# Optimization experiments

Measured on AMD Instinct MI355X. Metric: run time of the kernel, lower is better.

The kernel has to match this reference:

```python
import jax, jax.numpy as jnp
import numpy as np

HIDDEN = 512
NUM_HEADS = 8


def setup_inputs() -> dict:
    key = jax.random.key(0)
    ks = jax.random.split(key, 8)
    Tq, Tk, Cq, Ck, H = 1, 65536, 512, 512, HIDDEN
    s = 1.0 / np.sqrt(H)
    return {
        "Q": jax.random.normal(ks[0], (Tq, Cq), jnp.float32),
        "K": jax.random.normal(ks[1], (Tk, Ck), jnp.float32),
        "Wq": jax.random.normal(ks[2], (H, Cq), jnp.float32) * s,
        "bq": jax.random.normal(ks[3], (H,), jnp.float32) * s,
        "Wk": jax.random.normal(ks[4], (H, Ck), jnp.float32) * s,
        "bk": jax.random.normal(ks[5], (H,), jnp.float32) * s,
        "Wout": jax.random.normal(ks[6], (1, NUM_HEADS), jnp.float32) * 0.3,
        "bout": jax.random.normal(ks[7], (1,), jnp.float32) * 0.3,
    }


def reference(Q, K, Wq, bq, Wk, bk, Wout, bout):
    h = NUM_HEADS
    H = Wq.shape[0]
    d = H // h  # per-head dim
    # linear + ReLU projections
    Ql = jax.nn.relu(Q @ Wq.T + bq)          # [1, H]
    Kl = jax.nn.relu(K @ Wk.T + bk)          # [Tk, H]
    # split into heads (T_q == 1 is required by linear_out)
    Qh = Ql.reshape(h, d)                    # [h, d]
    Kh = Kl.reshape(-1, h, d)                # [Tk, h, d]
    # per-head scores, scaled by sqrt(d_head); dropout rate 0 -> identity
    scores = jnp.einsum('hd,thd->th', Qh, Kh) / (d ** 0.5)  # [Tk, h]
    # learned per-head fusion, then softmax over the T_k axis
    logits = scores @ Wout.T + bout          # [Tk, 1]
    return jax.nn.softmax(logits, axis=0)    # [Tk, 1]
```

## Files before the change

### kernel.cpp

```cpp
#include <hip/hip_runtime.h>
#include <hip/hip_fp16.h>

#define CDIM  512
#define ROWS  65536
#define NWG   128
#define TILES 16

typedef _Float16 half8  __attribute__((ext_vector_type(8)));
typedef _Float16 half4t __attribute__((ext_vector_type(4)));
typedef float    f32x16 __attribute__((ext_vector_type(16)));

__global__ void qproj_kernel(const float* __restrict__ Q, const float* __restrict__ Wq,
                             const float* __restrict__ bq, const float* __restrict__ Wout,
                             float* __restrict__ v) {
    __shared__ float qs[CDIM];
    const int t = threadIdx.x;
    qs[t] = Q[t]; qs[t + 256] = Q[t + 256];
    __syncthreads();
    const int jj  = t >> 4;
    const int sub = t & 15;
    const int j   = blockIdx.x * 16 + jj;
    const float4* w4 = (const float4*)(Wq + (size_t)j * CDIM + sub * 32);
    const float4* q4 = (const float4*)(qs + sub * 32);
    float s = 0.f;
    #pragma unroll
    for (int i = 0; i < 8; ++i) {
        float4 w = w4[i]; float4 q = q4[i];
        s = fmaf(w.x, q.x, s); s = fmaf(w.y, q.y, s);
        s = fmaf(w.z, q.z, s); s = fmaf(w.w, q.w, s);
    }
    s += __shfl_xor(s, 1); s += __shfl_xor(s, 2);
    s += __shfl_xor(s, 4); s += __shfl_xor(s, 8);
    if (sub == 0) {
        s += bq[j];
        s = fmaxf(s, 0.f);
        v[j] = s * Wout[j >> 6] * 0.125f;
    }
}

__global__ void wkfrag_kernel(const float* __restrict__ Wk, _Float16* __restrict__ Wkf) {
    const int gid = blockIdx.x * 256 + threadIdx.x;
    const int jb  = gid >> 11;
    const int kc  = (gid >> 6) & 31;
    const int l   = gid & 63;
    const int j   = jb * 32 + (l & 31);
    const int k   = kc * 16 + (l >> 5) * 8;
    const float* src = Wk + (size_t)j * CDIM + k;
    float4 f0 = *(const float4*)(src);
    float4 f1 = *(const float4*)(src + 4);
    half8 h;
    h[0]=(_Float16)f0.x; h[1]=(_Float16)f0.y; h[2]=(_Float16)f0.z; h[3]=(_Float16)f0.w;
    h[4]=(_Float16)f1.x; h[5]=(_Float16)f1.y; h[6]=(_Float16)f1.z; h[7]=(_Float16)f1.w;
    *(half8*)(Wkf + (size_t)gid * 8) = h;
}

__global__ __launch_bounds__(512, 2) void score_kernel(
    const float* __restrict__ Kmat, const _Float16* __restrict__ Wkf,
    const float* __restrict__ bk, const float* __restrict__ v,
    float* __restrict__ partial2)
{
    __shared__ alignas(16) char stage[2][32768];
    __shared__ float scratch[2][8][32];

    const int tid  = threadIdx.x;
    const int lane = tid & 63;
    const int wave = tid >> 6;
    const int l31  = lane & 31;
    const int lhi  = lane >> 5;
    const int cls  = blockIdx.y;
    const int jb   = cls * 8 + wave;

    half8 B[32];
    const half8* bsrc = (const half8*)Wkf + ((size_t)jb * 32) * 64 + lane;
    #pragma unroll
    for (int kc = 0; kc < 32; ++kc) B[kc] = bsrc[kc * 64];
    const int jmy = jb * 32 + l31;
    const float bj = bk[jmy];
    const float vj = v[jmy];

    const int rowbase0 = blockIdx.x * (TILES * 32);
    float* pbase = partial2 + (size_t)cls * ROWS;

    const int sw  = tid & 127;
    const int skc = sw >> 2;
    const int skh = (sw >> 1) & 1;
    const int spr = sw & 1;
    const int srow_off = tid >> 7;

    #pragma unroll
    for (int it = 0; it < 8; ++it) {
        const int row = it * 4 + srow_off;
        float4 g = *(const float4*)(Kmat + (size_t)(rowbase0 + row) * CDIM + sw * 4);
        half4t h = {(_Float16)g.x, (_Float16)g.y, (_Float16)g.z, (_Float16)g.w};
        const int off = skc * 1024 + (((row + 32 * skh + skc) & 63) * 16) + spr * 8;
        *(half4t*)(&stage[0][off]) = h;
    }
    __syncthreads();

    for (int t = 0; t < TILES; ++t) {
        const int cur = t & 1;
        const bool pf = (t + 1 < TILES);

        float4 g[8];
        if (pf) {
            const int rs = rowbase0 + (t + 1) * 32;
            #pragma unroll
            for (int it = 0; it < 8; ++it)
                g[it] = *(const float4*)(Kmat + (size_t)(rs + it * 4 + srow_off) * CDIM + sw * 4);
        }

        if (t > 0 && tid < 32) {
            float s = 0.f;
            #pragma unroll
            for (int w = 0; w < 8; ++w) s += scratch[(t - 1) & 1][w][tid];
            pbase[rowbase0 + (t - 1) * 32 + tid] = s;
        }

        f32x16 acc0, acc1;
        #pragma unroll
        for (int r = 0; r < 16; ++r) { acc0[r] = 0.f; acc1[r] = 0.f; }
        #pragma unroll
        for (int kc = 0; kc < 32; kc += 2) {
            half8 a0 = *(const half8*)(&stage[cur][kc * 1024 + ((lane + kc) & 63) * 16]);
            half8 a1 = *(const half8*)(&stage[cur][(kc + 1) * 1024 + ((lane + kc + 1) & 63) * 16]);
            acc0 = __builtin_amdgcn_mfma_f32_32x32x16_f16(a0, B[kc],     acc0, 0, 0, 0);
            acc1 = __builtin_amdgcn_mfma_f32_32x32x16_f16(a1, B[kc + 1], acc1, 0, 0, 0);
        }

        float part[16];
        #pragma unroll
        for (int r = 0; r < 16; ++r) {
            float x = fmaxf(acc0[r] + acc1[r] + bj, 0.f) * vj;
            x += __shfl_xor(x, 1);
            x += __shfl_xor(x, 2);
            x += __shfl_xor(x, 4);
            x += __shfl_xor(x, 8);
            x += __shfl_xor(x, 16);
            part[r] = x;
        }
        if (l31 == 0) {
            #pragma unroll
            for (int r = 0; r < 16; ++r)
                scratch[cur][wave][(r & 3) + 8 * (r >> 2) + 4 * lhi] = part[r];
        }

        if (pf) {
            #pragma unroll
            for (int it = 0; it < 8; ++it) {
                const int row = it * 4 + srow_off;
                half4t h = {(_Float16)g[it].x, (_Float16)g[it].y, (_Float16)g[it].z, (_Float16)g[it].w};
                const int off = skc * 1024 + (((row + 32 * skh + skc) & 63) * 16) + spr * 8;
                *(half4t*)(&stage[cur ^ 1][off]) = h;
            }
        }
        __syncthreads();
    }

    if (tid < 32) {
        float s = 0.f;
        #pragma unroll
        for (int w = 0; w < 8; ++w) s += scratch[(TILES - 1) & 1][w][tid];
        pbase[rowbase0 + (TILES - 1) * 32 + tid] = s;
    }
}

__global__ void expsum_kernel(const float* __restrict__ partial2, float* __restrict__ logits,
                              float* __restrict__ blocksum) {
    __shared__ float red[256];
    const int t = threadIdx.x;
    const int row = blockIdx.x * 256 + t;
    const float lg = partial2[row] + partial2[ROWS + row];
    logits[row] = lg;
    red[t] = expf(lg);
    __syncthreads();
    for (int s = 128; s > 0; s >>= 1) {
        if (t < s) red[t] += red[t + s];
        __syncthreads();
    }
    if (t == 0) blocksum[blockIdx.x] = red[0];
}

__global__ void norm_kernel(const float* __restrict__ logits, const float* __restrict__ blocksum,
                            float* __restrict__ out) {
    __shared__ float red[256];
    const int t = threadIdx.x;
    red[t] = blocksum[t];
    __syncthreads();
    for (int s = 128; s > 0; s >>= 1) {
        if (t < s) red[t] += red[t + s];
        __syncthreads();
    }
    const float zinv = 1.0f / red[0];
    const int i = blockIdx.x * 256 + t;
    out[i] = expf(logits[i]) * zinv;
}

extern "C" void kernel_launch(void* const* d_in, const int* in_sizes, int n_in,
                              void* d_out, int out_size, void* d_ws, size_t ws_size,
                              hipStream_t stream) {
    const float* Q    = (const float*)d_in[0];
    const float* Kmat = (const float*)d_in[1];
    const float* Wq   = (const float*)d_in[2];
    const float* bq   = (const float*)d_in[3];
    const float* Wk   = (const float*)d_in[4];
    const float* bk   = (const float*)d_in[5];
    const float* Wout = (const float*)d_in[6];
    float* out = (float*)d_out;

    char* ws = (char*)d_ws;
    _Float16* Wkf   = (_Float16*)(ws);
    float* v        = (float*)(ws + 524288);
    float* partial2 = (float*)(ws + 526336);
    float* logits   = (float*)(ws + 1050624);
    float* blocksum = (float*)(ws + 1312768);

    hipLaunchKernelGGL(qproj_kernel,  dim3(32),       dim3(256), 0, stream, Q, Wq, bq, Wout, v);
    hipLaunchKernelGGL(wkfrag_kernel, dim3(128),      dim3(256), 0, stream, Wk, Wkf);
    hipLaunchKernelGGL(score_kernel,  dim3(NWG, 2),   dim3(512), 0, stream, Kmat, Wkf, bk, v, partial2);
    hipLaunchKernelGGL(expsum_kernel, dim3(256),      dim3(256), 0, stream, partial2, logits, blocksum);
    hipLaunchKernelGGL(norm_kernel,   dim3(256),      dim3(256), 0, stream, logits, blocksum, out);
}
```

Before: 75.92 us.

## Stream fp32 K tiles directly into LDS via global_load_lds, convert at read

The score kernel's K-tile staging now uses 16-byte global_load_lds transfers that write fp32 rows straight into an XOR-swizzled shared-memory buffer. This replaces the old path of loading into registers, converting to fp16 and storing to LDS. Conversion to fp16 moves to the MFMA operand read, using packed round-toward-zero converts. The aim is to cut register pressure and VALU/LDS-store work in the prefetch path and let the async copy overlap with compute. In exchange, shared memory per block doubles to about 128KB, which limits occupancy to one block per CU, and LDS read traffic per MFMA doubles.

```diff
diff --git a/kernel.cpp b/kernel.cpp
--- a/kernel.cpp
+++ b/kernel.cpp
@@ -7,8 +7,12 @@
 #define TILES 16
 
 typedef _Float16 half8  __attribute__((ext_vector_type(8)));
-typedef _Float16 half4t __attribute__((ext_vector_type(4)));
+typedef __fp16   fp16x2 __attribute__((ext_vector_type(2)));
 typedef float    f32x16 __attribute__((ext_vector_type(16)));
+
+#define GLD_LDS16(gp, lp) __builtin_amdgcn_global_load_lds( \
+    (const __attribute__((address_space(1))) unsigned int*)(gp), \
+    (__attribute__((address_space(3))) unsigned int*)(lp), 16, 0, 0)
 
 __global__ void qproj_kernel(const float* __restrict__ Q, const float* __restrict__ Wq,
                              const float* __restrict__ bq, const float* __restrict__ Wout,
@@ -59,7 +63,7 @@
     const float* __restrict__ bk, const float* __restrict__ v,
     float* __restrict__ partial2)
 {
-    __shared__ alignas(16) char stage[2][32768];
+    __shared__ alignas(16) float stage[2][32 * 512];
     __shared__ float scratch[2][8][32];
 
     const int tid  = threadIdx.x;
@@ -81,32 +85,34 @@
     const int rowbase0 = blockIdx.x * (TILES * 32);
     float* pbase = partial2 + (size_t)cls * ROWS;
 
-    const int sw  = tid & 127;
-    const int skc = sw >> 2;
-    const int skh = (sw >> 1) & 1;
-    const int spr = sw & 1;
-    const int srow_off = tid >> 7;
-
-    #pragma unroll
-    for (int it = 0; it < 8; ++it) {
-        const int row = it * 4 + srow_off;
-        float4 g = *(const float4*)(Kmat + (size_t)(rowbase0 + row) * CDIM + sw * 4);
-        half4t h = {(_Float16)g.x, (_Float16)g.y, (_Float16)g.z, (_Float16)g.w};
-        const int off = skc * 1024 + (((row + 32 * skh + skc) & 63) * 16) + spr * 8;
-        *(half4t*)(&stage[0][off]) = h;
+    const int srow = wave >> 1;
+    const int scol = (wave & 1) << 6;
+
+    {
+        const float* tb = Kmat + (size_t)rowbase0 * CDIM;
+        #pragma unroll
+        for (int it = 0; it < 8; ++it) {
+            const int r = it * 4 + srow;
+            const int c = (scol + lane) ^ r;
+            GLD_LDS16(tb + (size_t)r * CDIM + c * 4,
+                      &stage[0][(it * 512 + wave * 64) * 4]);
+        }
     }
     __syncthreads();
 
     for (int t = 0; t < TILES; ++t) {
         const int cur = t & 1;
-        const bool pf = (t + 1 < TILES);
-
-        float4 g[8];
-        if (pf) {
-            const int rs = rowbase0 + (t + 1) * 32;
+
+        if (t + 1 < TILES) {
+            const float* tb = Kmat + (size_t)(rowbase0 + (t + 1) * 32) * CDIM;
+            float* db = &stage[cur ^ 1][0];
             #pragma unroll
-            for (int it = 0; it < 8; ++it)
-                g[it] = *(const float4*)(Kmat + (size_t)(rs + it * 4 + srow_off) * CDIM + sw * 4);
+            for (int it = 0; it < 8; ++it) {
+                const int r = it * 4 + srow;
+                const int c = (scol + lane) ^ r;
+                GLD_LDS16(tb + (size_t)r * CDIM + c * 4,
+                          db + (it * 512 + wave * 64) * 4);
+            }
         }
 
         if (t > 0 && tid < 32) {
@@ -116,15 +122,29 @@
             pbase[rowbase0 + (t - 1) * 32 + tid] = s;
         }
 
+        const float* sb = &stage[cur][0];
         f32x16 acc0, acc1;
         #pragma unroll
         for (int r = 0; r < 16; ++r) { acc0[r] = 0.f; acc1[r] = 0.f; }
         #pragma unroll
         for (int kc = 0; kc < 32; kc += 2) {
-            half8 a0 = *(const half8*)(&stage[cur][kc * 1024 + ((lane + kc) & 63) * 16]);
-            half8 a1 = *(const half8*)(&stage[cur][(kc + 1) * 1024 + ((lane + kc + 1) & 63) * 16]);
-            acc0 = __builtin_amdgcn_mfma_f32_32x32x16_f16(a0, B[kc],     acc0, 0, 0, 0);
-            acc1 = __builtin_amdgcn_mfma_f32_32x32x16_f16(a1, B[kc + 1], acc1, 0, 0, 0);
+            const int cb0 = kc * 4 + lhi * 2;
+            const int cb1 = cb0 + 4;
+            float4 f00 = *(const float4*)(sb + ((l31 * 128 + ((cb0    ) ^ l31)) << 2));
+            float4 f01 = *(const float4*)(sb + ((l31 * 128 + ((cb0 + 1) ^ l31)) << 2));
+            float4 f10 = *(const float4*)(sb + ((l31 * 128 + ((cb1    ) ^ l31)) << 2));
+            float4 f11 = *(const float4*)(sb + ((l31 * 128 + ((cb1 + 1) ^ l31)) << 2));
+            union { fp16x2 h2[4]; half8 h8; } u0, u1;
+            u0.h2[0] = __builtin_amdgcn_cvt_pkrtz(f00.x, f00.y);
+            u0.h2[1] = __builtin_amdgcn_cvt_pkrtz(f00.z, f00.w);
+            u0.h2[2] = __builtin_amdgcn_cvt_pkrtz(f01.x, f01.y);
+            u0.h2[3] = __builtin_amdgcn_cvt_pkrtz(f01.z, f01.w);
+            u1.h2[0] = __builtin_amdgcn_cvt_pkrtz(f10.x, f10.y);
+            u1.h2[1] = __builtin_amdgcn_cvt_pkrtz(f10.z, f10.w);
+            u1.h2[2] = __builtin_amdgcn_cvt_pkrtz(f11.x, f11.y);
+            u1.h2[3] = __builtin_amdgcn_cvt_pkrtz(f11.z, f11.w);
+            acc0 = __builtin_amdgcn_mfma_f32_32x32x16_f16(u0.h8, B[kc],     acc0, 0, 0, 0);
+            acc1 = __builtin_amdgcn_mfma_f32_32x32x16_f16(u1.h8, B[kc + 1], acc1, 0, 0, 0);
         }
 
         float part[16];
@@ -144,15 +164,6 @@
                 scratch[cur][wave][(r & 3) + 8 * (r >> 2) + 4 * lhi] = part[r];
         }
 
-        if (pf) {
-            #pragma unroll
-            for (int it = 0; it < 8; ++it) {
-                const int row = it * 4 + srow_off;
-                half4t h = {(_Float16)g[it].x, (_Float16)g[it].y, (_Float16)g[it].z, (_Float16)g[it].w};
-                const int off = skc * 1024 + (((row + 32 * skh + skc) & 63) * 16) + spr * 8;
-                *(half4t*)(&stage[cur ^ 1][off]) = h;
-            }
-        }
         __syncthreads();
     }
 
@@ -214,9 +225,9 @@
     float* logits   = (float*)(ws + 1050624);
     float* blocksum = (float*)(ws + 1312768);
 
-    hipLaunchKernelGGL(qproj_kernel,  dim3(32),       dim3(256), 0, stream, Q, Wq, bq, Wout, v);
-    hipLaunchKernelGGL(wkfrag_kernel, dim3(128),      dim3(256), 0, stream, Wk, Wkf);
-    hipLaunchKernelGGL(score_kernel,  dim3(NWG, 2),   dim3(512), 0, stream, Kmat, Wkf, bk, v, partial2);
-    hipLaunchKernelGGL(expsum_kernel, dim3(256),      dim3(256), 0, stream, partial2, logits, blocksum);
-    hipLaunchKernelGGL(norm_kernel,   dim3(256),      dim3(256), 0, stream, logits, blocksum, out);
-}
+    hipLaunchKernelGGL(qproj_kernel,  dim3(32),     dim3(256), 0, stream, Q, Wq, bq, Wout, v);
+    hipLaunchKernelGGL(wkfrag_kernel, dim3(128),    dim3(256), 0, stream, Wk, Wkf);
+    hipLaunchKernelGGL(score_kernel,  dim3(NWG, 2), dim3(512), 0, stream, Kmat, Wkf, bk, v, partial2);
+    hipLaunchKernelGGL(expsum_kernel, dim3(256),    dim3(256), 0, stream, partial2, logits, blocksum);
+    hipLaunchKernelGGL(norm_kernel,   dim3(256),    dim3(256), 0, stream, logits, blocksum, out);
+}
```

Measured after the change: 107.0 us. 40.9% more time.

## Split score kernel into 4 column groups of 4 waves with row-major swizzled staging

Applied to the files above, without the earlier changes.

Changes the score kernel from 2 column groups of 8 waves to 4 groups of 4 waves (256 threads), so each block handles 128 hidden columns and the K tile is staged 4 times instead of twice. Staging now uses a row-major fp16 layout with XOR swizzle and packed cvt_pkrtz conversion, and the next-tile prefetch is split into two halves interleaved with the MFMA loop using sched barriers. The cross-lane reduction becomes a transpose-style butterfly that needs fewer shuffles. The cost is twice the global K reads and conversions, plus a fourth partial buffer that expsum must add.

```diff
diff --git a/kernel.cpp b/kernel.cpp
--- a/kernel.cpp
+++ b/kernel.cpp
@@ -3,11 +3,12 @@
 
 #define CDIM  512
 #define ROWS  65536
-#define NWG   128
 #define TILES 16
+#define GX    128
+#define NCLS  4
 
 typedef _Float16 half8  __attribute__((ext_vector_type(8)));
-typedef _Float16 half4t __attribute__((ext_vector_type(4)));
+typedef __fp16   fp16x2 __attribute__((ext_vector_type(2)));
 typedef float    f32x16 __attribute__((ext_vector_type(16)));
 
 __global__ void qproj_kernel(const float* __restrict__ Q, const float* __restrict__ Wq,
@@ -54,13 +55,13 @@
     *(half8*)(Wkf + (size_t)gid * 8) = h;
 }
 
-__global__ __launch_bounds__(512, 2) void score_kernel(
+__global__ __launch_bounds__(256, 2) void score_kernel(
     const float* __restrict__ Kmat, const _Float16* __restrict__ Wkf,
     const float* __restrict__ bk, const float* __restrict__ v,
     float* __restrict__ partial2)
 {
-    __shared__ alignas(16) char stage[2][32768];
-    __shared__ float scratch[2][8][32];
+    __shared__ alignas(16) _Float16 stage[2][32][512];
+    __shared__ float scratch2[2][4][32];
 
     const int tid  = threadIdx.x;
     const int lane = tid & 63;
@@ -68,32 +69,34 @@
     const int l31  = lane & 31;
     const int lhi  = lane >> 5;
     const int cls  = blockIdx.y;
-    const int jb   = cls * 8 + wave;
+    const int jb   = cls * 4 + wave;
 
     half8 B[32];
-    const half8* bsrc = (const half8*)Wkf + ((size_t)jb * 32) * 64 + lane;
+    const half8* bsrc = (const half8*)Wkf + (size_t)jb * 2048 + lane;
     #pragma unroll
     for (int kc = 0; kc < 32; ++kc) B[kc] = bsrc[kc * 64];
     const int jmy = jb * 32 + l31;
     const float bj = bk[jmy];
     const float vj = v[jmy];
 
-    const int rowbase0 = blockIdx.x * (TILES * 32);
+    const int rowbase = blockIdx.x * (TILES * 32);
     float* pbase = partial2 + (size_t)cls * ROWS;
 
-    const int sw  = tid & 127;
-    const int skc = sw >> 2;
-    const int skh = (sw >> 1) & 1;
-    const int spr = sw & 1;
-    const int srow_off = tid >> 7;
-
-    #pragma unroll
-    for (int it = 0; it < 8; ++it) {
-        const int row = it * 4 + srow_off;
-        float4 g = *(const float4*)(Kmat + (size_t)(rowbase0 + row) * CDIM + sw * 4);
-        half4t h = {(_Float16)g.x, (_Float16)g.y, (_Float16)g.z, (_Float16)g.w};
-        const int off = skc * 1024 + (((row + 32 * skh + skc) & 63) * 16) + spr * 8;
-        *(half4t*)(&stage[0][off]) = h;
+    {
+        #pragma unroll
+        for (int i = 0; i < 8; ++i) {
+            const int rt = wave * 8 + i;
+            const float* src = Kmat + (size_t)(rowbase + rt) * CDIM + lane * 8;
+            float4 a = *(const float4*)(src);
+            float4 b = *(const float4*)(src + 4);
+            union { fp16x2 h2[4]; half8 h8; } u;
+            u.h2[0] = __builtin_amdgcn_cvt_pkrtz(a.x, a.y);
+            u.h2[1] = __builtin_amdgcn_cvt_pkrtz(a.z, a.w);
+            u.h2[2] = __builtin_amdgcn_cvt_pkrtz(b.x, b.y);
+            u.h2[3] = __builtin_amdgcn_cvt_pkrtz(b.z, b.w);
+            const int slot = lane ^ (rt & 7);
+            *(half8*)(&stage[0][rt][slot * 8]) = u.h8;
+        }
     }
     __syncthreads();
 
@@ -101,66 +104,142 @@
         const int cur = t & 1;
         const bool pf = (t + 1 < TILES);
 
-        float4 g[8];
+        if (t > 0 && tid < 32) {
+            const int pt = (t - 1) & 1;
+            float s = scratch2[pt][0][tid] + scratch2[pt][1][tid]
+                    + scratch2[pt][2][tid] + scratch2[pt][3][tid];
+            pbase[rowbase + (t - 1) * 32 + tid] = s;
+        }
+
+        f32x16 acc0, acc1;
+        #pragma unroll
+        for (int r = 0; r < 16; ++r) { acc0[r] = 0.f; acc1[r] = 0.f; }
+
+        const _Float16* sb = &stage[cur][0][0];
+
+        float4 ga0[4], gb0[4];
         if (pf) {
-            const int rs = rowbase0 + (t + 1) * 32;
+            const int rs = rowbase + (t + 1) * 32;
             #pragma unroll
-            for (int it = 0; it < 8; ++it)
-                g[it] = *(const float4*)(Kmat + (size_t)(rs + it * 4 + srow_off) * CDIM + sw * 4);
-        }
-
-        if (t > 0 && tid < 32) {
-            float s = 0.f;
-            #pragma unroll
-            for (int w = 0; w < 8; ++w) s += scratch[(t - 1) & 1][w][tid];
-            pbase[rowbase0 + (t - 1) * 32 + tid] = s;
-        }
-
-        f32x16 acc0, acc1;
-        #pragma unroll
-        for (int r = 0; r < 16; ++r) { acc0[r] = 0.f; acc1[r] = 0.f; }
-        #pragma unroll
-        for (int kc = 0; kc < 32; kc += 2) {
-            half8 a0 = *(const half8*)(&stage[cur][kc * 1024 + ((lane + kc) & 63) * 16]);
-            half8 a1 = *(const half8*)(&stage[cur][(kc + 1) * 1024 + ((lane + kc + 1) & 63) * 16]);
+            for (int i = 0; i < 4; ++i) {
+                const float* src = Kmat + (size_t)(rs + wave * 8 + i) * CDIM + lane * 8;
+                ga0[i] = *(const float4*)(src);
+                gb0[i] = *(const float4*)(src + 4);
+            }
+        }
+        __builtin_amdgcn_sched_barrier(0);
+
+        #pragma unroll
+        for (int kc = 0; kc < 16; kc += 2) {
+            const int ch0 = (kc * 2 + lhi) ^ (l31 & 7);
+            const int ch1 = ((kc + 1) * 2 + lhi) ^ (l31 & 7);
+            half8 a0 = *(const half8*)(sb + l31 * 512 + ch0 * 8);
+            half8 a1 = *(const half8*)(sb + l31 * 512 + ch1 * 8);
             acc0 = __builtin_amdgcn_mfma_f32_32x32x16_f16(a0, B[kc],     acc0, 0, 0, 0);
             acc1 = __builtin_amdgcn_mfma_f32_32x32x16_f16(a1, B[kc + 1], acc1, 0, 0, 0);
         }
 
-        float part[16];
-        #pragma unroll
-        for (int r = 0; r < 16; ++r) {
-            float x = fmaxf(acc0[r] + acc1[r] + bj, 0.f) * vj;
-            x += __shfl_xor(x, 1);
-            x += __shfl_xor(x, 2);
-            x += __shfl_xor(x, 4);
-            x += __shfl_xor(x, 8);
-            x += __shfl_xor(x, 16);
-            part[r] = x;
-        }
-        if (l31 == 0) {
-            #pragma unroll
-            for (int r = 0; r < 16; ++r)
-                scratch[cur][wave][(r & 3) + 8 * (r >> 2) + 4 * lhi] = part[r];
-        }
-
         if (pf) {
             #pragma unroll
-            for (int it = 0; it < 8; ++it) {
-                const int row = it * 4 + srow_off;
-                half4t h = {(_Float16)g[it].x, (_Float16)g[it].y, (_Float16)g[it].z, (_Float16)g[it].w};
-                const int off = skc * 1024 + (((row + 32 * skh + skc) & 63) * 16) + spr * 8;
-                *(half4t*)(&stage[cur ^ 1][off]) = h;
+            for (int i = 0; i < 4; ++i) {
+                const int rt = wave * 8 + i;
+                union { fp16x2 h2[4]; half8 h8; } u;
+                u.h2[0] = __builtin_amdgcn_cvt_pkrtz(ga0[i].x, ga0[i].y);
+                u.h2[1] = __builtin_amdgcn_cvt_pkrtz(ga0[i].z, ga0[i].w);
+                u.h2[2] = __builtin_amdgcn_cvt_pkrtz(gb0[i].x, gb0[i].y);
+                u.h2[3] = __builtin_amdgcn_cvt_pkrtz(gb0[i].z, gb0[i].w);
+                const int slot = lane ^ (rt & 7);
+                *(half8*)(&stage[cur ^ 1][rt][slot * 8]) = u.h8;
             }
         }
+
+        float4 ga1[4], gb1[4];
+        if (pf) {
+            const int rs = rowbase + (t + 1) * 32;
+            #pragma unroll
+            for (int i = 0; i < 4; ++i) {
+                const float* src = Kmat + (size_t)(rs + wave * 8 + 4 + i) * CDIM + lane * 8;
+                ga1[i] = *(const float4*)(src);
+                gb1[i] = *(const float4*)(src + 4);
+            }
+        }
+        __builtin_amdgcn_sched_barrier(0);
+
+        #pragma unroll
+        for (int kc = 16; kc < 32; kc += 2) {
+            const int ch0 = (kc * 2 + lhi) ^ (l31 & 7);
+            const int ch1 = ((kc + 1) * 2 + lhi) ^ (l31 & 7);
+            half8 a0 = *(const half8*)(sb + l31 * 512 + ch0 * 8);
+            half8 a1 = *(const half8*)(sb + l31 * 512 + ch1 * 8);
+            acc0 = __builtin_amdgcn_mfma_f32_32x32x16_f16(a0, B[kc],     acc0, 0, 0, 0);
+            acc1 = __builtin_amdgcn_mfma_f32_32x32x16_f16(a1, B[kc + 1], acc1, 0, 0, 0);
+        }
+
+        if (pf) {
+            #pragma unroll
+            for (int i = 0; i < 4; ++i) {
+                const int rt = wave * 8 + 4 + i;
+                union { fp16x2 h2[4]; half8 h8; } u;
+                u.h2[0] = __builtin_amdgcn_cvt_pkrtz(ga1[i].x, ga1[i].y);
+                u.h2[1] = __builtin_amdgcn_cvt_pkrtz(ga1[i].z, ga1[i].w);
+                u.h2[2] = __builtin_amdgcn_cvt_pkrtz(gb1[i].x, gb1[i].y);
+                u.h2[3] = __builtin_amdgcn_cvt_pkrtz(gb1[i].z, gb1[i].w);
+                const int slot = lane ^ (rt & 7);
+                *(half8*)(&stage[cur ^ 1][rt][slot * 8]) = u.h8;
+            }
+        }
+
+        float x[16];
+        #pragma unroll
+        for (int r = 0; r < 16; ++r)
+            x[r] = fmaxf(acc0[r] + acc1[r] + bj, 0.f) * vj;
+
+        float q0[8];
+        #pragma unroll
+        for (int i = 0; i < 8; ++i) {
+            const bool b = lane & 1;
+            float keep = b ? x[i + 8] : x[i];
+            float send = b ? x[i] : x[i + 8];
+            q0[i] = keep + __shfl_xor(send, 1);
+        }
+        float q1[4];
+        #pragma unroll
+        for (int i = 0; i < 4; ++i) {
+            const bool b = lane & 2;
+            float keep = b ? q0[i + 4] : q0[i];
+            float send = b ? q0[i] : q0[i + 4];
+            q1[i] = keep + __shfl_xor(send, 2);
+        }
+        float q2[2];
+        #pragma unroll
+        for (int i = 0; i < 2; ++i) {
+            const bool b = lane & 4;
+            float keep = b ? q1[i + 2] : q1[i];
+            float send = b ? q1[i] : q1[i + 2];
+            q2[i] = keep + __shfl_xor(send, 4);
+        }
+        float q3;
+        {
+            const bool b = lane & 8;
+            float keep = b ? q2[1] : q2[0];
+            float send = b ? q2[0] : q2[1];
+            q3 = keep + __shfl_xor(send, 8);
+        }
+        float s = q3 + __shfl_xor(q3, 16);
+        if (l31 < 16) {
+            const int r   = ((l31 & 1) << 3) | ((l31 & 2) << 1) | ((l31 & 4) >> 1) | ((l31 & 8) >> 3);
+            const int row = (r & 3) + 8 * (r >> 2) + 4 * lhi;
+            scratch2[cur][wave][row] = s;
+        }
+
         __syncthreads();
     }
 
     if (tid < 32) {
-        float s = 0.f;
-        #pragma unroll
-        for (int w = 0; w < 8; ++w) s += scratch[(TILES - 1) & 1][w][tid];
-        pbase[rowbase0 + (TILES - 1) * 32 + tid] = s;
+        const int pt = (TILES - 1) & 1;
+        float s = scratch2[pt][0][tid] + scratch2[pt][1][tid]
+                + scratch2[pt][2][tid] + scratch2[pt][3][tid];
+        pbase[rowbase + (TILES - 1) * 32 + tid] = s;
     }
 }
 
@@ -169,7 +248,8 @@
     __shared__ float red[256];
     const int t = threadIdx.x;
     const int row = blockIdx.x * 256 + t;
-    const float lg = partial2[row] + partial2[ROWS + row];
+    const float lg = partial2[row] + partial2[ROWS + row]
+                   + partial2[2 * ROWS + row] + partial2[3 * ROWS + row];
     logits[row] = lg;
     red[t] = expf(lg);
     __syncthreads();
@@ -211,12 +291,12 @@
     _Float16* Wkf   = (_Float16*)(ws);
     float* v        = (float*)(ws + 524288);
     float* partial2 = (float*)(ws + 526336);
-    float* logits   = (float*)(ws + 1050624);
-    float* blocksum = (float*)(ws + 1312768);
-
-    hipLaunchKernelGGL(qproj_kernel,  dim3(32),       dim3(256), 0, stream, Q, Wq, bq, Wout, v);
-    hipLaunchKernelGGL(wkfrag_kernel, dim3(128),      dim3(256), 0, stream, Wk, Wkf);
-    hipLaunchKernelGGL(score_kernel,  dim3(NWG, 2),   dim3(512), 0, stream, Kmat, Wkf, bk, v, partial2);
-    hipLaunchKernelGGL(expsum_kernel, dim3(256),      dim3(256), 0, stream, partial2, logits, blocksum);
-    hipLaunchKernelGGL(norm_kernel,   dim3(256),      dim3(256), 0, stream, logits, blocksum, out);
-}
+    float* logits   = (float*)(ws + 1574912);
+    float* blocksum = (float*)(ws + 1837056);
+
+    hipLaunchKernelGGL(qproj_kernel,  dim3(32),        dim3(256), 0, stream, Q, Wq, bq, Wout, v);
+    hipLaunchKernelGGL(wkfrag_kernel, dim3(128),       dim3(256), 0, stream, Wk, Wkf);
+    hipLaunchKernelGGL(score_kernel,  dim3(GX, NCLS),  dim3(256), 0, stream, Kmat, Wkf, bk, v, partial2);
+    hipLaunchKernelGGL(expsum_kernel, dim3(256),       dim3(256), 0, stream, partial2, logits, blocksum);
+    hipLaunchKernelGGL(norm_kernel,   dim3(256),       dim3(256), 0, stream, logits, blocksum, out);
+}
```

New measurement: 64.43 us. 15.1% less time.

## Hold K rows in registers and stream Wk fragments through LDS via direct loads

Applied to the files above, without the earlier changes.

Restructures the score kernel so each wave keeps 32 rows of converted K as MFMA A-operands in registers and swaps 64KB halves of the fp16 Wk fragment matrix into LDS with global_load_lds, instead of keeping Wk in registers and staging K tiles through LDS. Each block now handles 512 rows for one 256-column half, so each wave processes 64 rows in two passes and alternates Wk halves to reuse what is already loaded. The per-row shuffle reduction becomes a transposing butterfly tree that needs fewer shuffles, and fp32-to-fp16 conversion uses packed cvt_pkrtz. The cost is 128KB of LDS per block, which limits occupancy, plus round-toward-zero conversion and less overlap between K loads and compute.

```diff
diff --git a/kernel.cpp b/kernel.cpp
--- a/kernel.cpp
+++ b/kernel.cpp
@@ -1,14 +1,25 @@
 #include <hip/hip_runtime.h>
 #include <hip/hip_fp16.h>
 
-#define CDIM  512
-#define ROWS  65536
-#define NWG   128
-#define TILES 16
+#define CDIM 512
+#define ROWS 65536
 
 typedef _Float16 half8  __attribute__((ext_vector_type(8)));
-typedef _Float16 half4t __attribute__((ext_vector_type(4)));
+typedef __fp16   fp16x2 __attribute__((ext_vector_type(2)));
 typedef float    f32x16 __attribute__((ext_vector_type(16)));
+
+#define GLD_LDS16(gp, lp) __builtin_amdgcn_global_load_lds( \
+    (const __attribute__((address_space(1))) unsigned int*)(gp), \
+    (__attribute__((address_space(3))) unsigned int*)(lp), 16, 0, 0)
+
+__device__ __forceinline__ half8 cvt8(float4 f0, float4 f1) {
+    union { fp16x2 h2[4]; half8 h8; } u;
+    u.h2[0] = __builtin_amdgcn_cvt_pkrtz(f0.x, f0.y);
+    u.h2[1] = __builtin_amdgcn_cvt_pkrtz(f0.z, f0.w);
+    u.h2[2] = __builtin_amdgcn_cvt_pkrtz(f1.x, f1.y);
+    u.h2[3] = __builtin_amdgcn_cvt_pkrtz(f1.z, f1.w);
+    return u.h8;
+}
 
 __global__ void qproj_kernel(const float* __restrict__ Q, const float* __restrict__ Wq,
                              const float* __restrict__ bq, const float* __restrict__ Wout,
@@ -48,10 +59,7 @@
     const float* src = Wk + (size_t)j * CDIM + k;
     float4 f0 = *(const float4*)(src);
     float4 f1 = *(const float4*)(src + 4);
-    half8 h;
-    h[0]=(_Float16)f0.x; h[1]=(_Float16)f0.y; h[2]=(_Float16)f0.z; h[3]=(_Float16)f0.w;
-    h[4]=(_Float16)f1.x; h[5]=(_Float16)f1.y; h[6]=(_Float16)f1.z; h[7]=(_Float16)f1.w;
-    *(half8*)(Wkf + (size_t)gid * 8) = h;
+    *(half8*)(Wkf + (size_t)gid * 8) = cvt8(f0, f1);
 }
 
 __global__ __launch_bounds__(512, 2) void score_kernel(
@@ -59,109 +67,115 @@
     const float* __restrict__ bk, const float* __restrict__ v,
     float* __restrict__ partial2)
 {
-    __shared__ alignas(16) char stage[2][32768];
-    __shared__ float scratch[2][8][32];
+    __shared__ alignas(16) char Blds[131072];
 
     const int tid  = threadIdx.x;
     const int lane = tid & 63;
     const int wave = tid >> 6;
     const int l31  = lane & 31;
     const int lhi  = lane >> 5;
-    const int cls  = blockIdx.y;
-    const int jb   = cls * 8 + wave;
-
-    half8 B[32];
-    const half8* bsrc = (const half8*)Wkf + ((size_t)jb * 32) * 64 + lane;
+    const int bid  = blockIdx.x;
+    const int cls  = bid & 1;
+    const int rowblock = bid >> 1;
+
+    const int wrow = rowblock * 512 + wave * 64;
+    float* pbase = partial2 + (size_t)cls * ROWS;
+
+    const char* wkf0 = (const char*)Wkf + (size_t)(cls * 8 + 0) * 32768;
+    const char* wkf1 = (const char*)Wkf + (size_t)(cls * 8 + 4) * 32768;
+
+#define SWAPB(src) { \
+    _Pragma("unroll") for (int i = 0; i < 16; ++i) \
+        GLD_LDS16((src) + (size_t)i * 8192 + tid * 16, Blds + i * 8192 + tid * 16); }
+
+    half8 a[32];
+#define LOADA(rb) { \
+    const float* ab = Kmat + (size_t)((rb) + l31) * CDIM + lhi * 8;       \
+    _Pragma("unroll") for (int g = 0; g < 8; ++g) {                        \
+        float4 f[8];                                                       \
+        _Pragma("unroll") for (int q = 0; q < 4; ++q) {                    \
+            f[2*q]   = *(const float4*)(ab + (g*4+q) * 16);                \
+            f[2*q+1] = *(const float4*)(ab + (g*4+q) * 16 + 4);            \
+        }                                                                  \
+        _Pragma("unroll") for (int q = 0; q < 4; ++q)                      \
+            a[g*4+q] = cvt8(f[2*q], f[2*q+1]);                             \
+    } }
+
+    float part[16];
+
+#define DOPHASE(h) { \
+    for (int jbl = 0; jbl < 4; ++jbl) {                                             \
+        const int jg = cls * 256 + (h) * 128 + jbl * 32 + l31;                      \
+        const float bj = bk[jg];                                                    \
+        const float vj = v[jg];                                                     \
+        f32x16 acc0, acc1;                                                          \
+        _Pragma("unroll") for (int r = 0; r < 16; ++r) { acc0[r] = 0.f; acc1[r] = 0.f; } \
+        _Pragma("unroll") for (int kc = 0; kc < 32; kc += 2) {                      \
+            half8 b0 = *(const half8*)(Blds + (((jbl*32 + kc    ) * 64 + lane) << 4)); \
+            half8 b1 = *(const half8*)(Blds + (((jbl*32 + kc + 1) * 64 + lane) << 4)); \
+            acc0 = __builtin_amdgcn_mfma_f32_32x32x16_f16(a[kc],     b0, acc0, 0, 0, 0); \
+            acc1 = __builtin_amdgcn_mfma_f32_32x32x16_f16(a[kc + 1], b1, acc1, 0, 0, 0); \
+        }                                                                           \
+        _Pragma("unroll") for (int r = 0; r < 16; ++r)                              \
+            part[r] += fmaxf(acc0[r] + acc1[r] + bj, 0.f) * vj;                     \
+    } }
+
+#define TREESTORE(dst) { \
+    float q0[8];                                                                    \
+    _Pragma("unroll") for (int i = 0; i < 8; ++i) {                                 \
+        const bool b = lane & 1;                                                    \
+        float keep = b ? part[i + 8] : part[i];                                     \
+        float send = b ? part[i] : part[i + 8];                                     \
+        q0[i] = keep + __shfl_xor(send, 1);                                         \
+    }                                                                               \
+    float q1[4];                                                                    \
+    _Pragma("unroll") for (int i = 0; i < 4; ++i) {                                 \
+        const bool b = lane & 2;                                                    \
+        float keep = b ? q0[i + 4] : q0[i];                                         \
+        float send = b ? q0[i] : q0[i + 4];                                         \
+        q1[i] = keep + __shfl_xor(send, 2);                                         \
+    }                                                                               \
+    float q2[2];                                                                    \
+    _Pragma("unroll") for (int i = 0; i < 2; ++i) {                                 \
+        const bool b = lane & 4;                                                    \
+        float keep = b ? q1[i + 2] : q1[i];                                         \
+        float send = b ? q1[i] : q1[i + 2];                                         \
+        q2[i] = keep + __shfl_xor(send, 4);                                         \
+    }                                                                               \
+    float q3;                                                                       \
+    { const bool b = lane & 8;                                                      \
+      float keep = b ? q2[1] : q2[0];                                               \
+      float send = b ? q2[0] : q2[1];                                               \
+      q3 = keep + __shfl_xor(send, 8); }                                            \
+    float s = q3 + __shfl_xor(q3, 16);                                              \
+    if (l31 < 16) {                                                                 \
+        const int rr  = ((l31 & 1) << 3) | ((l31 & 2) << 1) | ((l31 & 4) >> 1) | ((l31 & 8) >> 3); \
+        const int row = (rr & 3) + 8 * (rr >> 2) + 4 * lhi;                         \
+        (dst)[row] = s;                                                             \
+    } }
+
+    SWAPB(wkf0);
+    LOADA(wrow);
+    __syncthreads();
+
     #pragma unroll
-    for (int kc = 0; kc < 32; ++kc) B[kc] = bsrc[kc * 64];
-    const int jmy = jb * 32 + l31;
-    const float bj = bk[jmy];
-    const float vj = v[jmy];
-
-    const int rowbase0 = blockIdx.x * (TILES * 32);
-    float* pbase = partial2 + (size_t)cls * ROWS;
-
-    const int sw  = tid & 127;
-    const int skc = sw >> 2;
-    const int skh = (sw >> 1) & 1;
-    const int spr = sw & 1;
-    const int srow_off = tid >> 7;
-
+    for (int r = 0; r < 16; ++r) part[r] = 0.f;
+    DOPHASE(0);
+    __syncthreads();
+    SWAPB(wkf1);
+    __syncthreads();
+    DOPHASE(1);
+    TREESTORE(pbase + wrow);
+
+    LOADA(wrow + 32);
     #pragma unroll
-    for (int it = 0; it < 8; ++it) {
-        const int row = it * 4 + srow_off;
-        float4 g = *(const float4*)(Kmat + (size_t)(rowbase0 + row) * CDIM + sw * 4);
-        half4t h = {(_Float16)g.x, (_Float16)g.y, (_Float16)g.z, (_Float16)g.w};
-        const int off = skc * 1024 + (((row + 32 * skh + skc) & 63) * 16) + spr * 8;
-        *(half4t*)(&stage[0][off]) = h;
-    }
-    __syncthreads();
-
-    for (int t = 0; t < TILES; ++t) {
-        const int cur = t & 1;
-        const bool pf = (t + 1 < TILES);
-
-        float4 g[8];
-        if (pf) {
-            const int rs = rowbase0 + (t + 1) * 32;
-            #pragma unroll
-            for (int it = 0; it < 8; ++it)
-                g[it] = *(const float4*)(Kmat + (size_t)(rs + it * 4 + srow_off) * CDIM + sw * 4);
-        }
-
-        if (t > 0 && tid < 32) {
-            float s = 0.f;
-            #pragma unroll
-            for (int w = 0; w < 8; ++w) s += scratch[(t - 1) & 1][w][tid];
-            pbase[rowbase0 + (t - 1) * 32 + tid] = s;
-        }
-
-        f32x16 acc0, acc1;
-        #pragma unroll
-        for (int r = 0; r < 16; ++r) { acc0[r] = 0.f; acc1[r] = 0.f; }
-        #pragma unroll
-        for (int kc = 0; kc < 32; kc += 2) {
-            half8 a0 = *(const half8*)(&stage[cur][kc * 1024 + ((lane + kc) & 63) * 16]);
-            half8 a1 = *(const half8*)(&stage[cur][(kc + 1) * 1024 + ((lane + kc + 1) & 63) * 16]);
-            acc0 = __builtin_amdgcn_mfma_f32_32x32x16_f16(a0, B[kc],     acc0, 0, 0, 0);
-            acc1 = __builtin_amdgcn_mfma_f32_32x32x16_f16(a1, B[kc + 1], acc1, 0, 0, 0);
-        }
-
-        float part[16];
-        #pragma unroll
-        for (int r = 0; r < 16; ++r) {
-            float x = fmaxf(acc0[r] + acc1[r] + bj, 0.f) * vj;
-            x += __shfl_xor(x, 1);
-            x += __shfl_xor(x, 2);
-            x += __shfl_xor(x, 4);
-            x += __shfl_xor(x, 8);
-            x += __shfl_xor(x, 16);
-            part[r] = x;
-        }
-        if (l31 == 0) {
-            #pragma unroll
-            for (int r = 0; r < 16; ++r)
-                scratch[cur][wave][(r & 3) + 8 * (r >> 2) + 4 * lhi] = part[r];
-        }
-
-        if (pf) {
-            #pragma unroll
-            for (int it = 0; it < 8; ++it) {
-                const int row = it * 4 + srow_off;
-                half4t h = {(_Float16)g[it].x, (_Float16)g[it].y, (_Float16)g[it].z, (_Float16)g[it].w};
-                const int off = skc * 1024 + (((row + 32 * skh + skc) & 63) * 16) + spr * 8;
-                *(half4t*)(&stage[cur ^ 1][off]) = h;
-            }
-        }
-        __syncthreads();
-    }
-
-    if (tid < 32) {
-        float s = 0.f;
-        #pragma unroll
-        for (int w = 0; w < 8; ++w) s += scratch[(TILES - 1) & 1][w][tid];
-        pbase[rowbase0 + (TILES - 1) * 32 + tid] = s;
-    }
+    for (int r = 0; r < 16; ++r) part[r] = 0.f;
+    DOPHASE(1);
+    __syncthreads();
+    SWAPB(wkf0);
+    __syncthreads();
+    DOPHASE(0);
+    TREESTORE(pbase + wrow + 32);
 }
 
 __global__ void expsum_kernel(const float* __restrict__ partial2, float* __restrict__ logits,
@@ -214,9 +228,9 @@
     float* logits   = (float*)(ws + 1050624);
     float* blocksum = (float*)(ws + 1312768);
 
-    hipLaunchKernelGGL(qproj_kernel,  dim3(32),       dim3(256), 0, stream, Q, Wq, bq, Wout, v);
-    hipLaunchKernelGGL(wkfrag_kernel, dim3(128),      dim3(256), 0, stream, Wk, Wkf);
-    hipLaunchKernelGGL(score_kernel,  dim3(NWG, 2),   dim3(512), 0, stream, Kmat, Wkf, bk, v, partial2);
-    hipLaunchKernelGGL(expsum_kernel, dim3(256),      dim3(256), 0, stream, partial2, logits, blocksum);
-    hipLaunchKernelGGL(norm_kernel,   dim3(256),      dim3(256), 0, stream, logits, blocksum, out);
-}
+    hipLaunchKernelGGL(qproj_kernel,  dim3(32),   dim3(256), 0, stream, Q, Wq, bq, Wout, v);
+    hipLaunchKernelGGL(wkfrag_kernel, dim3(128),  dim3(256), 0, stream, Wk, Wkf);
+    hipLaunchKernelGGL(score_kernel,  dim3(256),  dim3(512), 0, stream, Kmat, Wkf, bk, v, partial2);
+    hipLaunchKernelGGL(expsum_kernel, dim3(256),  dim3(256), 0, stream, partial2, logits, blocksum);
+    hipLaunchKernelGGL(norm_kernel,   dim3(256),  dim3(256), 0, stream, logits, blocksum, out);
+}
```

Result: slower. 92.73 us (+22.2%).
